# Optimization experiments

Measured on AMD Instinct MI355X. Metric: run time of the kernel, lower is better.

## Reference

```python
import jax, jax.numpy as jnp
import numpy as np

B, N, T, L = 4, 512, 288, 128
NEG_SLOPE = 0.2
TEMPERATURE = 0.2
CLAMP = 10.0
EPS = 1e-10


def setup_inputs() -> dict:
    key = jax.random.key(0)
    ks = jax.random.split(key, 6)
    s_in = 1.0 / np.sqrt(T)
    s_lat = 1.0 / np.sqrt(2 * L)
    s_b = 1.0 / np.sqrt(L)
    x = jax.random.normal(ks[0], (B, N, T), dtype=jnp.float32)
    W1 = jax.random.normal(ks[1], (L, T), dtype=jnp.float32) * s_in
    W2 = jax.random.normal(ks[2], (L, T), dtype=jnp.float32) * s_in
    Wp = jax.random.normal(ks[3], (L, 2 * L), dtype=jnp.float32) * s_lat
    Wb = jax.random.normal(ks[4], (L,), dtype=jnp.float32) * s_b
    noise = jnp.clip(jax.random.uniform(ks[5], (N, N), dtype=jnp.float32), 1e-6, 1.0 - 1e-6)
    return {
        "x": x,
        "W1": W1, "b1": jnp.zeros((L,), jnp.float32),
        "W2": W2, "b2": jnp.zeros((L,), jnp.float32),
        "Wp": Wp, "bp": jnp.zeros((L,), jnp.float32),
        "Wb": Wb, "bb": jnp.zeros((1,), jnp.float32),
        "noise": noise,
    }


def _leaky(v):
    return jnp.where(v >= 0, v, NEG_SLOPE * v)


def reference(x, W1, b1, W2, b2, Wp, bp, Wb, bb, noise):
    # per-node projections (B, N, L)
    x1 = _leaky(jnp.einsum('bnt,lt->bnl', x, W1) + b1)
    x2 = _leaky(jnp.einsum('bnt,lt->bnl', x, W2) + b2)
    # linear_para_latent(cat(x1_i, x2_j)) == x1_i @ Wp_a^T + x2_j @ Wp_b^T + bp
    Wp_a, Wp_b = Wp[:, :L], Wp[:, L:]
    s1 = jnp.einsum('bnl,ml->bnm', x1, Wp_a)  # (B, N, L_out)
    s2 = jnp.einsum('bnl,ml->bnm', x2, Wp_b)
    pair = s1[:, :, None, :] + s2[:, None, :, :] + bp  # (B, N, N, L)
    h = _leaky(pair)
    logits = jnp.einsum('bijl,l->bij', h, Wb) + bb[0]  # (B, N, N)
    p = jax.nn.sigmoid(logits).mean(axis=0)            # (N, N)
    p = p * (1.0 - jnp.eye(N, dtype=p.dtype))          # fill_diagonal_(0)
    # relaxed Bernoulli sample (binary concrete) with logit clamping
    logit_p = jnp.clip(jnp.log(p + EPS) - jnp.log1p(-p + EPS), -CLAMP, CLAMP)
    logistic = jnp.log(noise) - jnp.log1p(-noise)
    adj = jax.nn.sigmoid((logit_p + logistic) / TEMPERATURE)
    return adj
```

## Files before the change

kernel.cpp:

```cpp
#include <hip/hip_runtime.h>
#include <hip/hip_bf16.h>
#include <math.h>

#define NN 512
#define NT 288

__global__ __launch_bounds__(256) void kT(
    const float* __restrict__ W1, const float* __restrict__ W2,
    const float* __restrict__ Wp,
    float* __restrict__ Wt, float* __restrict__ Wpt)
{
    int g = blockIdx.x * 256 + threadIdx.x;
    if (g < 288 * 256) {
        int k = g >> 8, col = g & 255;
        Wt[g] = (col < 128) ? W1[col * 288 + k] : W2[(col - 128) * 288 + k];
    } else {
        int h = g - 288 * 256;
        int k = h >> 8, col = h & 255;
        Wpt[h] = (col < 128) ? Wp[col * 256 + k]
                             : Wp[(col - 128) * 256 + 128 + k];
    }
}

__global__ __launch_bounds__(512) void kP(
    const float* __restrict__ x,
    const float* __restrict__ Wt,
    const float* __restrict__ b1,
    const float* __restrict__ b2,
    const float* __restrict__ Wpt,
    const float* __restrict__ bp,
    const float* __restrict__ Wb,
    const float* __restrict__ bb,
    float* __restrict__ S12,
    float* __restrict__ Aarr,
    float* __restrict__ Carr)
{
    __shared__ __align__(16) float xs[8 * NT];
    __shared__ __align__(16) float x12s[8 * 256];
    __shared__ __align__(16) float ph[8 * 256];

    const int t   = threadIdx.x;
    const int bn0 = blockIdx.x * 8;
    const int col = t & 255;
    const int kh  = t >> 8;

    for (int q = 0; q < 2; ++q) {
        int idx = q * 512 + t;
        if (idx < 576) {
            int row = idx / 72, c4 = idx % 72;
            *(float4*)&xs[row * NT + c4 * 4] =
                *(const float4*)&x[(size_t)(bn0 + row) * NT + c4 * 4];
        }
    }
    __syncthreads();

    const float* wtb = Wt + kh * 144 * 256 + col;
    const int kb1 = kh * 144;
    const float bias1 = (col < 128) ? b1[col] : b2[col - 128];

    float acc[8];
#pragma unroll
    for (int n = 0; n < 8; ++n) acc[n] = 0.0f;

#pragma unroll 1
    for (int k4 = 0; k4 < 36; ++k4) {
        float w0 = wtb[(k4 * 4 + 0) * 256];
        float w1 = wtb[(k4 * 4 + 1) * 256];
        float w2 = wtb[(k4 * 4 + 2) * 256];
        float w3 = wtb[(k4 * 4 + 3) * 256];
#pragma unroll
        for (int n = 0; n < 8; ++n) {
            float4 xv = *(const float4*)&xs[n * NT + kb1 + k4 * 4];
            acc[n] = fmaf(w0, xv.x, acc[n]);
            acc[n] = fmaf(w1, xv.y, acc[n]);
            acc[n] = fmaf(w2, xv.z, acc[n]);
            acc[n] = fmaf(w3, xv.w, acc[n]);
        }
    }
    if (kh) {
#pragma unroll
        for (int n = 0; n < 8; ++n) ph[n * 256 + col] = acc[n];
    }
    __syncthreads();
    if (!kh) {
#pragma unroll
        for (int n = 0; n < 8; ++n) {
            float v = acc[n] + ph[n * 256 + col] + bias1;
            x12s[n * 256 + col] = fmaxf(v, 0.2f * v);
        }
    }
    __syncthreads();

    const int koff = (col < 128) ? 0 : 128;
    const float* wptb = Wpt + kh * 64 * 256 + col;
    const float bias2 = (col < 128) ? bp[col] : 0.0f;
    const int kb2 = koff + kh * 64;

    float acc2[8];
#pragma unroll
    for (int n = 0; n < 8; ++n) acc2[n] = 0.0f;

#pragma unroll 1
    for (int k4 = 0; k4 < 16; ++k4) {
        float w0 = wptb[(k4 * 4 + 0) * 256];
        float w1 = wptb[(k4 * 4 + 1) * 256];
        float w2 = wptb[(k4 * 4 + 2) * 256];
        float w3 = wptb[(k4 * 4 + 3) * 256];
#pragma unroll
        for (int n = 0; n < 8; ++n) {
            float4 xv = *(const float4*)&x12s[n * 256 + kb2 + k4 * 4];
            acc2[n] = fmaf(w0, xv.x, acc2[n]);
            acc2[n] = fmaf(w1, xv.y, acc2[n]);
            acc2[n] = fmaf(w2, xv.z, acc2[n]);
            acc2[n] = fmaf(w3, xv.w, acc2[n]);
        }
    }
    if (kh) {
#pragma unroll
        for (int n = 0; n < 8; ++n) ph[n * 256 + col] = acc2[n];
    }
    __syncthreads();

    float* s12s = xs;
    if (!kh) {
#pragma unroll
        for (int n = 0; n < 8; ++n) {
            float sv = acc2[n] + ph[n * 256 + col] + bias2;
            S12[(size_t)(bn0 + n) * 256 + col] = sv;
            s12s[n * 257 + col] = sv;
        }
    }
    __syncthreads();

    {
        int lane32 = t & 31;
        int n = (t >> 5) & 7;
        int isC = t >> 8;
        int base = isC ? 128 : 0;
        float sum = 0.0f;
#pragma unroll
        for (int s = 0; s < 4; ++s) {
            int j = lane32 + s * 32;
            sum = fmaf(s12s[n * 257 + base + j], Wb[j], sum);
        }
#pragma unroll
        for (int m = 16; m >= 1; m >>= 1)
            sum += __shfl_xor(sum, m, 32);
        if (lane32 == 0) {
            if (isC) Carr[bn0 + n] = 0.6f * sum;
            else     Aarr[bn0 + n] = 0.6f * sum + bb[0];
        }
    }
}

__global__ __launch_bounds__(512) void kQ(
    const float* __restrict__ S12,
    const float* __restrict__ Aarr,
    const float* __restrict__ Carr,
    const float* __restrict__ Wb,
    const float* __restrict__ noise,
    float* __restrict__ out)
{
    __shared__ __align__(16) float smem[32768];
    float* S1t = smem;
    float* S2t = smem + 16384;

    const int t = threadIdx.x;
    const int bx = blockIdx.x, by = blockIdx.y;

#pragma unroll
    for (int q = 0; q < 16; ++q) {
        int task = q * 512 + t;
        int isS2 = task >> 12;
        int r    = task & 4095;
        int bz   = r >> 10;
        int row  = (r >> 5) & 31;
        int c4   = r & 31;
        size_t src = (size_t)(bz * NN + (isS2 ? by : bx) * 32 + row) * 256
                     + (isS2 ? 128 : 0) + c4 * 4;
        float4 v = *(const float4*)&S12[src];
        float* dst = (isS2 ? S2t : S1t) + bz * 4096;
        int rw = row ^ ((c4 & 7) << 2);
        dst[(c4 * 4 + 0) * 32 + rw] = v.x;
        dst[(c4 * 4 + 1) * 32 + rw] = v.y;
        dst[(c4 * 4 + 2) * 32 + rw] = v.z;
        dst[(c4 * 4 + 3) * 32 + rw] = v.w;
    }
    __syncthreads();

    const int lh = t >> 8;
    const int bz = (t >> 6) & 3;
    const int s  = t & 63;
    const int i0 = (s >> 3) << 2, j0 = (s & 7) << 2;

    const float* S1b = S1t + bz * 4096 + lh * 64 * 32;
    const float* S2b = S2t + bz * 4096 + lh * 64 * 32;
    const float* wbp = Wb + lh * 64;

    float accv[16];
#pragma unroll
    for (int k = 0; k < 16; ++k) accv[k] = 0.0f;

    for (int l4 = 0; l4 < 16; ++l4) {
        const int sw = (l4 & 7) << 2;
        const int lrow = l4 * 4 * 32;
        float4 wv = *(const float4*)&wbp[l4 * 4];
        const float wl[4] = {wv.x, wv.y, wv.z, wv.w};
#pragma unroll
        for (int d = 0; d < 4; ++d) {
            float4 a = *(const float4*)&S1b[lrow + d * 32 + (i0 ^ sw)];
            float4 b = *(const float4*)&S2b[lrow + d * 32 + (j0 ^ sw)];
            float w = wl[d];
            float ai[4] = {a.x, a.y, a.z, a.w};
            float bj[4] = {b.x, b.y, b.z, b.w};
#pragma unroll
            for (int ii = 0; ii < 4; ++ii)
#pragma unroll
                for (int jj = 0; jj < 4; ++jj) {
                    float tv = ai[ii] + bj[jj];
                    accv[ii * 4 + jj] = fmaf(fabsf(tv), w, accv[ii * 4 + jj]);
                }
        }
    }

    float* red = smem;
    const int tid2 = t & 255;
    __syncthreads();
    if (lh) {
#pragma unroll
        for (int q = 0; q < 4; ++q) {
            float4 v = {accv[4 * q], accv[4 * q + 1], accv[4 * q + 2], accv[4 * q + 3]};
            *(float4*)&red[q * 1024 + tid2 * 4] = v;
        }
    }
    __syncthreads();

    float sig[16];
    if (!lh) {
#pragma unroll
        for (int q = 0; q < 4; ++q) {
            float4 v = *(const float4*)&red[q * 1024 + tid2 * 4];
            accv[4 * q]     += v.x;
            accv[4 * q + 1] += v.y;
            accv[4 * q + 2] += v.z;
            accv[4 * q + 3] += v.w;
        }
        float Av[4], Cv[4];
#pragma unroll
        for (int ii = 0; ii < 4; ++ii) Av[ii] = Aarr[bz * NN + bx * 32 + i0 + ii];
#pragma unroll
        for (int jj = 0; jj < 4; ++jj) Cv[jj] = Carr[bz * NN + by * 32 + j0 + jj];
#pragma unroll
        for (int ii = 0; ii < 4; ++ii)
#pragma unroll
            for (int jj = 0; jj < 4; ++jj) {
                float lg = Av[ii] + Cv[jj] + 0.4f * accv[ii * 4 + jj];
                sig[ii * 4 + jj] = 1.0f / (1.0f + expf(-lg));
            }
        float* redB = smem + 4096;
        if (bz) {
#pragma unroll
            for (int q = 0; q < 4; ++q) {
                float4 v = {sig[4 * q], sig[4 * q + 1], sig[4 * q + 2], sig[4 * q + 3]};
                *(float4*)&redB[(bz - 1) * 1024 + q * 256 + s * 4] = v;
            }
        }
    }
    __syncthreads();

    float* redB = smem + 4096;
    float* redP = smem + 7168;
    if (t < 64) {
#pragma unroll
        for (int bzz = 0; bzz < 3; ++bzz)
#pragma unroll
            for (int q = 0; q < 4; ++q) {
                float4 v = *(const float4*)&redB[bzz * 1024 + q * 256 + t * 4];
                sig[4 * q]     += v.x;
                sig[4 * q + 1] += v.y;
                sig[4 * q + 2] += v.z;
                sig[4 * q + 3] += v.w;
            }
#pragma unroll
        for (int q = 0; q < 4; ++q) {
            float4 v = {sig[4 * q], sig[4 * q + 1], sig[4 * q + 2], sig[4 * q + 3]};
            *(float4*)&redP[t * 16 + q * 4] = v;
        }
    }
    __syncthreads();

    if (t < 256) {
        int i   = t >> 3;
        int j0f = (t & 7) * 4;
        int sP  = (t >> 5) * 8 + (t & 7);
        int k0  = ((t >> 3) & 3) * 4;
        float4 pv4 = *(const float4*)&redP[sP * 16 + k0];
        float pv[4] = {pv4.x, pv4.y, pv4.z, pv4.w};

        int gi = bx * 32 + i;
        size_t base = (size_t)gi * NN + by * 32 + j0f;
        float4 nz = *(const float4*)&noise[base];
        float nv[4] = {nz.x, nz.y, nz.z, nz.w};

        float4 o;
        float* op = (float*)&o;
#pragma unroll
        for (int c = 0; c < 4; ++c) {
            float p = 0.25f * pv[c];
            int gj = by * 32 + j0f + c;
            if (gj == gi) p = 0.0f;
            float lp = logf(p + 1e-10f) - log1pf(-p + 1e-10f);
            lp = fminf(fmaxf(lp, -10.0f), 10.0f);
            float lgs = logf(nv[c]) - log1pf(-nv[c]);
            op[c] = 1.0f / (1.0f + expf(-(lp + lgs) * 5.0f));
        }
        *(float4*)&out[base] = o;
    }
}

extern "C" void kernel_launch(void* const* d_in, const int* in_sizes, int n_in,
                              void* d_out, int out_size, void* d_ws, size_t ws_size,
                              hipStream_t stream) {
    const float* x     = (const float*)d_in[0];
    const float* W1    = (const float*)d_in[1];
    const float* b1    = (const float*)d_in[2];
    const float* W2    = (const float*)d_in[3];
    const float* b2    = (const float*)d_in[4];
    const float* Wp    = (const float*)d_in[5];
    const float* bp    = (const float*)d_in[6];
    const float* Wb    = (const float*)d_in[7];
    const float* bb    = (const float*)d_in[8];
    const float* noise = (const float*)d_in[9];

    float* ws   = (float*)d_ws;
    float* S12  = ws;
    float* Aarr = ws + 524288;
    float* Carr = Aarr + 2048;
    float* Wt   = Carr + 2048;
    float* Wpt  = Wt + 73728;

    kT<<<416, 256, 0, stream>>>(W1, W2, Wp, Wt, Wpt);
    kP<<<256, 512, 0, stream>>>(x, Wt, b1, b2, Wpt, bp, Wb, bb,
                                S12, Aarr, Carr);
    kQ<<<dim3(16, 16), 512, 0, stream>>>(S12, Aarr, Carr, Wb, noise,
                                         (float*)d_out);
}
```

Before: 45.42 us.

## Register-tile projection GEMMs 8x4 per thread with 8-way K split

Restructures the per-node projection kernel so each thread computes an 8-row by 4-column output tile using float4 weight loads, with the K dimension split across 8 thread groups instead of 2. Partial sums are reduced through a larger shared buffer by one group. This raises arithmetic intensity per load and vectorizes global and shared memory accesses. The cost is more shared memory, a serial 7-way reduction in one warp group, and idle threads during the reduction phase.

Result: faster. 38.29 us, median of 2 (-15.7%).

```diff
diff --git a/kernel.cpp b/kernel.cpp
--- a/kernel.cpp
+++ b/kernel.cpp
@@ -37,97 +37,148 @@
 {
     __shared__ __align__(16) float xs[8 * NT];
     __shared__ __align__(16) float x12s[8 * 256];
-    __shared__ __align__(16) float ph[8 * 256];
+    __shared__ __align__(16) float ph[7 * 2048];
+    __shared__ __align__(16) float s12s[8 * 260];
 
     const int t   = threadIdx.x;
     const int bn0 = blockIdx.x * 8;
-    const int col = t & 255;
-    const int kh  = t >> 8;
+    const int c4  = t & 63;
+    const int khe = t >> 6;
 
     for (int q = 0; q < 2; ++q) {
         int idx = q * 512 + t;
         if (idx < 576) {
-            int row = idx / 72, c4 = idx % 72;
-            *(float4*)&xs[row * NT + c4 * 4] =
-                *(const float4*)&x[(size_t)(bn0 + row) * NT + c4 * 4];
-        }
-    }
-    __syncthreads();
-
-    const float* wtb = Wt + kh * 144 * 256 + col;
-    const int kb1 = kh * 144;
-    const float bias1 = (col < 128) ? b1[col] : b2[col - 128];
-
-    float acc[8];
-#pragma unroll
-    for (int n = 0; n < 8; ++n) acc[n] = 0.0f;
-
-#pragma unroll 1
-    for (int k4 = 0; k4 < 36; ++k4) {
-        float w0 = wtb[(k4 * 4 + 0) * 256];
-        float w1 = wtb[(k4 * 4 + 1) * 256];
-        float w2 = wtb[(k4 * 4 + 2) * 256];
-        float w3 = wtb[(k4 * 4 + 3) * 256];
-#pragma unroll
-        for (int n = 0; n < 8; ++n) {
-            float4 xv = *(const float4*)&xs[n * NT + kb1 + k4 * 4];
-            acc[n] = fmaf(w0, xv.x, acc[n]);
-            acc[n] = fmaf(w1, xv.y, acc[n]);
-            acc[n] = fmaf(w2, xv.z, acc[n]);
-            acc[n] = fmaf(w3, xv.w, acc[n]);
-        }
-    }
-    if (kh) {
-#pragma unroll
-        for (int n = 0; n < 8; ++n) ph[n * 256 + col] = acc[n];
-    }
-    __syncthreads();
-    if (!kh) {
-#pragma unroll
-        for (int n = 0; n < 8; ++n) {
-            float v = acc[n] + ph[n * 256 + col] + bias1;
-            x12s[n * 256 + col] = fmaxf(v, 0.2f * v);
-        }
-    }
-    __syncthreads();
-
-    const int koff = (col < 128) ? 0 : 128;
-    const float* wptb = Wpt + kh * 64 * 256 + col;
-    const float bias2 = (col < 128) ? bp[col] : 0.0f;
-    const int kb2 = koff + kh * 64;
-
-    float acc2[8];
-#pragma unroll
-    for (int n = 0; n < 8; ++n) acc2[n] = 0.0f;
-
-#pragma unroll 1
-    for (int k4 = 0; k4 < 16; ++k4) {
-        float w0 = wptb[(k4 * 4 + 0) * 256];
-        float w1 = wptb[(k4 * 4 + 1) * 256];
-        float w2 = wptb[(k4 * 4 + 2) * 256];
-        float w3 = wptb[(k4 * 4 + 3) * 256];
-#pragma unroll
-        for (int n = 0; n < 8; ++n) {
-            float4 xv = *(const float4*)&x12s[n * 256 + kb2 + k4 * 4];
-            acc2[n] = fmaf(w0, xv.x, acc2[n]);
-            acc2[n] = fmaf(w1, xv.y, acc2[n]);
-            acc2[n] = fmaf(w2, xv.z, acc2[n]);
-            acc2[n] = fmaf(w3, xv.w, acc2[n]);
-        }
-    }
-    if (kh) {
-#pragma unroll
-        for (int n = 0; n < 8; ++n) ph[n * 256 + col] = acc2[n];
-    }
-    __syncthreads();
-
-    float* s12s = xs;
-    if (!kh) {
-#pragma unroll
-        for (int n = 0; n < 8; ++n) {
-            float sv = acc2[n] + ph[n * 256 + col] + bias2;
-            S12[(size_t)(bn0 + n) * 256 + col] = sv;
-            s12s[n * 257 + col] = sv;
+            int row = idx / 72, cc = idx % 72;
+            *(float4*)&xs[row * NT + cc * 4] =
+                *(const float4*)&x[(size_t)(bn0 + row) * NT + cc * 4];
+        }
+    }
+    __syncthreads();
+
+    float acc[8][4];
+#pragma unroll
+    for (int n = 0; n < 8; ++n)
+#pragma unroll
+        for (int c = 0; c < 4; ++c) acc[n][c] = 0.0f;
+
+    const int kbase1 = khe * 36;
+#pragma unroll 2
+    for (int k4 = 0; k4 < 9; ++k4) {
+        const int k0 = kbase1 + k4 * 4;
+        float4 w0 = *(const float4*)&Wt[(size_t)(k0 + 0) * 256 + c4 * 4];
+        float4 w1 = *(const float4*)&Wt[(size_t)(k0 + 1) * 256 + c4 * 4];
+        float4 w2 = *(const float4*)&Wt[(size_t)(k0 + 2) * 256 + c4 * 4];
+        float4 w3 = *(const float4*)&Wt[(size_t)(k0 + 3) * 256 + c4 * 4];
+        const float* w0p = (const float*)&w0;
+        const float* w1p = (const float*)&w1;
+        const float* w2p = (const float*)&w2;
+        const float* w3p = (const float*)&w3;
+#pragma unroll
+        for (int n = 0; n < 8; ++n) {
+            float4 xv = *(const float4*)&xs[n * NT + k0];
+#pragma unroll
+            for (int c = 0; c < 4; ++c) {
+                acc[n][c] = fmaf(xv.x, w0p[c], acc[n][c]);
+                acc[n][c] = fmaf(xv.y, w1p[c], acc[n][c]);
+                acc[n][c] = fmaf(xv.z, w2p[c], acc[n][c]);
+                acc[n][c] = fmaf(xv.w, w3p[c], acc[n][c]);
+            }
+        }
+    }
+
+    if (khe) {
+#pragma unroll
+        for (int n = 0; n < 8; ++n) {
+            float4 v = {acc[n][0], acc[n][1], acc[n][2], acc[n][3]};
+            *(float4*)&ph[(khe - 1) * 2048 + n * 256 + c4 * 4] = v;
+        }
+    }
+    __syncthreads();
+    if (!khe) {
+        float4 bias4 = (c4 < 32) ? *(const float4*)&b1[c4 * 4]
+                                 : *(const float4*)&b2[(c4 - 32) * 4];
+        const float* bp4 = (const float*)&bias4;
+#pragma unroll
+        for (int n = 0; n < 8; ++n) {
+            float s0 = acc[n][0], s1 = acc[n][1], s2 = acc[n][2], s3 = acc[n][3];
+#pragma unroll
+            for (int p = 0; p < 7; ++p) {
+                float4 v = *(const float4*)&ph[p * 2048 + n * 256 + c4 * 4];
+                s0 += v.x; s1 += v.y; s2 += v.z; s3 += v.w;
+            }
+            float4 r;
+            float* rp = (float*)&r;
+            float sv[4] = {s0, s1, s2, s3};
+#pragma unroll
+            for (int c = 0; c < 4; ++c) {
+                float v = sv[c] + bp4[c];
+                rp[c] = fmaxf(v, 0.2f * v);
+            }
+            *(float4*)&x12s[n * 256 + c4 * 4] = r;
+        }
+    }
+    __syncthreads();
+
+    float acc2[8][4];
+#pragma unroll
+    for (int n = 0; n < 8; ++n)
+#pragma unroll
+        for (int c = 0; c < 4; ++c) acc2[n][c] = 0.0f;
+
+    const int koff = (c4 < 32) ? 0 : 128;
+    const int kbase2 = khe * 16;
+#pragma unroll 2
+    for (int k4 = 0; k4 < 4; ++k4) {
+        const int k0 = kbase2 + k4 * 4;
+        float4 w0 = *(const float4*)&Wpt[(size_t)(k0 + 0) * 256 + c4 * 4];
+        float4 w1 = *(const float4*)&Wpt[(size_t)(k0 + 1) * 256 + c4 * 4];
+        float4 w2 = *(const float4*)&Wpt[(size_t)(k0 + 2) * 256 + c4 * 4];
+        float4 w3 = *(const float4*)&Wpt[(size_t)(k0 + 3) * 256 + c4 * 4];
+        const float* w0p = (const float*)&w0;
+        const float* w1p = (const float*)&w1;
+        const float* w2p = (const float*)&w2;
+        const float* w3p = (const float*)&w3;
+#pragma unroll
+        for (int n = 0; n < 8; ++n) {
+            float4 xv = *(const float4*)&x12s[n * 256 + koff + k0];
+#pragma unroll
+            for (int c = 0; c < 4; ++c) {
+                acc2[n][c] = fmaf(xv.x, w0p[c], acc2[n][c]);
+                acc2[n][c] = fmaf(xv.y, w1p[c], acc2[n][c]);
+                acc2[n][c] = fmaf(xv.z, w2p[c], acc2[n][c]);
+                acc2[n][c] = fmaf(xv.w, w3p[c], acc2[n][c]);
+            }
+        }
+    }
+
+    if (khe) {
+#pragma unroll
+        for (int n = 0; n < 8; ++n) {
+            float4 v = {acc2[n][0], acc2[n][1], acc2[n][2], acc2[n][3]};
+            *(float4*)&ph[(khe - 1) * 2048 + n * 256 + c4 * 4] = v;
+        }
+    }
+    __syncthreads();
+    if (!khe) {
+        float4 bias4;
+        if (c4 < 32) bias4 = *(const float4*)&bp[c4 * 4];
+        else         bias4 = make_float4(0.f, 0.f, 0.f, 0.f);
+        const float* bp4 = (const float*)&bias4;
+#pragma unroll
+        for (int n = 0; n < 8; ++n) {
+            float s0 = acc2[n][0], s1 = acc2[n][1], s2 = acc2[n][2], s3 = acc2[n][3];
+#pragma unroll
+            for (int p = 0; p < 7; ++p) {
+                float4 v = *(const float4*)&ph[p * 2048 + n * 256 + c4 * 4];
+                s0 += v.x; s1 += v.y; s2 += v.z; s3 += v.w;
+            }
+            float sv[4] = {s0, s1, s2, s3};
+            float4 r;
+            float* rp = (float*)&r;
+#pragma unroll
+            for (int c = 0; c < 4; ++c) rp[c] = sv[c] + bp4[c];
+            *(float4*)&S12[(size_t)(bn0 + n) * 256 + c4 * 4] = r;
+            *(float4*)&s12s[n * 260 + c4 * 4] = r;
         }
     }
     __syncthreads();
@@ -141,7 +192,7 @@
 #pragma unroll
         for (int s = 0; s < 4; ++s) {
             int j = lane32 + s * 32;
-            sum = fmaf(s12s[n * 257 + base + j], Wb[j], sum);
+            sum = fmaf(s12s[n * 260 + base + j], Wb[j], sum);
         }
 #pragma unroll
         for (int m = 16; m >= 1; m >>= 1)
```
